# Kernel optimization log

Hardware: AMD Instinct MI355X
Metric: run time of the kernel (lower is better)

Reference implementation:

```python
import jax, jax.numpy as jnp
import numpy as np

B, T, D, H, O = 16, 2048, 512, 512, 256  # batch, max seq len, input, hidden, output


def setup_inputs() -> dict:
    key = jax.random.key(0)
    ks = jax.random.split(key, 12)
    x = jax.random.normal(ks[0], (B, T, D), dtype=jnp.float32)
    # ragged lengths: zero-pad the tail of each sample (zero rows => masked out)
    lengths = jax.random.randint(ks[1], (B,), T // 4, T + 1)
    valid = jnp.arange(T)[None, :] < lengths[:, None]
    x = x * valid[:, :, None].astype(x.dtype)
    s = float(1.0 / np.sqrt(H))  # PyTorch LSTM init range
    u = lambda k, shape: jax.random.uniform(k, shape, jnp.float32, -s, s)
    return {
        "x": x,
        "W_ih0": u(ks[2], (4 * H, D)), "W_hh0": u(ks[3], (4 * H, H)),
        "b_ih0": u(ks[4], (4 * H,)),   "b_hh0": u(ks[5], (4 * H,)),
        "W_ih1": u(ks[6], (4 * H, H)), "W_hh1": u(ks[7], (4 * H, H)),
        "b_ih1": u(ks[8], (4 * H,)),   "b_hh1": u(ks[9], (4 * H,)),
        "W_fc": u(ks[10], (O, H)),     "b_fc": u(ks[11], (O,)),
    }


def _lstm_layer(seq, mask, Wih, Whh, bih, bhh):
    """Masked LSTM layer over full batch.

    Skipping masked steps (state carried through unchanged) is mathematically
    identical to running the LSTM on the filtered (non-zero-row) subsequence,
    which is what the original per-sample Python loop computes.
    seq: [B, T, in], mask: [B, T] bool. Returns (outputs [B,T,H], h_final [B,H]).
    """
    Bn, Hn = seq.shape[0], Whh.shape[1]
    h0 = jnp.zeros((Bn, Hn), seq.dtype)
    c0 = jnp.zeros((Bn, Hn), seq.dtype)

    def step(carry, inp):
        h, c = carry
        x_t, m_t = inp
        gates = x_t @ Wih.T + bih + h @ Whh.T + bhh  # [B, 4H]
        i, f, g, o = jnp.split(gates, 4, axis=-1)    # PyTorch gate order i,f,g,o
        i = jax.nn.sigmoid(i)
        f = jax.nn.sigmoid(f)
        g = jnp.tanh(g)
        o = jax.nn.sigmoid(o)
        c_new = f * c + i * g
        h_new = o * jnp.tanh(c_new)
        m = m_t[:, None]
        h = jnp.where(m, h_new, h)
        c = jnp.where(m, c_new, c)
        return (h, c), h

    (hT, _), outs = jax.lax.scan(step, (h0, c0), (seq.transpose(1, 0, 2), mask.T))
    return outs.transpose(1, 0, 2), hT


def reference(x, W_ih0, W_hh0, b_ih0, b_hh0, W_ih1, W_hh1, b_ih1, b_hh1, W_fc, b_fc):
    mask = jnp.sum(x, axis=2) != 0  # [B, T] rows kept by the original filter
    seq1, _ = _lstm_layer(x, mask, W_ih0, W_hh0, b_ih0, b_hh0)
    _, hT = _lstm_layer(seq1, mask, W_ih1, W_hh1, b_ih1, b_hh1)
    return hT @ W_fc.T + b_fc  # [B, O]
```

## Files before the change

kernel.cpp:

```cpp
#include <hip/hip_runtime.h>

typedef _Float16 h16;
typedef __attribute__((ext_vector_type(2))) _Float16 h16x2;
typedef __attribute__((ext_vector_type(4))) _Float16 h16x4;
typedef __attribute__((ext_vector_type(8))) _Float16 h16x8;
typedef __attribute__((ext_vector_type(4))) float    f32x4;
typedef __attribute__((ext_vector_type(4))) unsigned u32x4;
typedef __attribute__((ext_vector_type(2))) unsigned u32x2;

constexpr int B_  = 16;
constexpr int T_  = 2048;
constexpr int D_  = 512;
constexpr int H_  = 512;
constexpr int O_  = 256;
constexpr int G4_ = 2048;
constexpr int BT_ = B_ * T_;

__device__ __forceinline__ float sigm(float x)   { return 1.f / (1.f + __expf(-x)); }
__device__ __forceinline__ float tanh_f(float x) { return 1.f - 2.f / (1.f + __expf(2.f * x)); }

__device__ __forceinline__ u32x4 load_cg16(const unsigned* p) {
  u32x4 r;
  asm volatile("global_load_dwordx4 %0, %1, off sc0 sc1" : "=v"(r) : "v"(p) : "memory");
  return r;
}

__global__ void k_prep_x(const float* __restrict__ x, h16* __restrict__ Xh,
                         unsigned* __restrict__ maskbits) {
  const int row = blockIdx.x;
  const int b = row >> 11, t = row & 2047;
  const float2* xr = (const float2*)(x + (size_t)row * D_);
  float2 v = xr[threadIdx.x];
  h16x2 hv = { (h16)v.x, (h16)v.y };
  *(h16x2*)(Xh + (size_t)row * D_ + threadIdx.x * 2) = hv;
  float s = v.x + v.y;
  #pragma unroll
  for (int off = 32; off > 0; off >>= 1) s += __shfl_down(s, off, 64);
  __shared__ float red[4];
  const int lane = threadIdx.x & 63, wv = threadIdx.x >> 6;
  if (lane == 0) red[wv] = s;
  __syncthreads();
  if (threadIdx.x == 0) {
    float tot = red[0] + red[1] + red[2] + red[3];
    if (tot != 0.f) atomicOr(&maskbits[t], 1u << b);
  }
}

__global__ void k_cvt(const float* __restrict__ s, h16* __restrict__ d, int n4) {
  int i = blockIdx.x * 256 + threadIdx.x;
  if (i < n4) {
    f32x4 v = ((const f32x4*)s)[i];
    h16x4 o = { (h16)v.x, (h16)v.y, (h16)v.z, (h16)v.w };
    ((h16x4*)d)[i] = o;
  }
}

__global__ void k_bias(const float* __restrict__ a, const float* __restrict__ b,
                       float* __restrict__ o, int n) {
  int i = blockIdx.x * 256 + threadIdx.x;
  if (i < n) o[i] = a[i] + b[i];
}

__global__ __launch_bounds__(256, 2)
void k_gemm(const h16* __restrict__ A, const h16* __restrict__ Bm, h16* __restrict__ C,
            int M, int N, int K) {
  __shared__ h16 As[128 * 32];
  __shared__ h16 Bs[128 * 32];
  const int tiles_n = N >> 7;
  const int tm = blockIdx.x / tiles_n, tn = blockIdx.x % tiles_n;
  const int tid = threadIdx.x, lane = tid & 63, wv = tid >> 6;
  const int wm = (wv >> 1) * 64, wn = (wv & 1) * 64;
  const int ml = lane & 15, qd = lane >> 4;
  f32x4 acc[4][4] = {};
  const h16* Arow = A + (size_t)(tm * 128) * K;
  const h16* Brow = Bm + (size_t)(tn * 128) * K;
  for (int kt = 0; kt < K; kt += 32) {
    __syncthreads();
    #pragma unroll
    for (int p = 0; p < 2; ++p) {
      int ch = tid + p * 256;
      int r = ch >> 2, qq = ch & 3;
      int sidx = r * 4 + ((qq + r) & 3);
      *(h16x8*)(As + sidx * 8) = *(const h16x8*)(Arow + (size_t)r * K + kt + qq * 8);
      *(h16x8*)(Bs + sidx * 8) = *(const h16x8*)(Brow + (size_t)r * K + kt + qq * 8);
    }
    __syncthreads();
    h16x8 af[4], bfv[4];
    #pragma unroll
    for (int i = 0; i < 4; ++i) {
      int ra = wm + i * 16 + ml;
      af[i]  = *(const h16x8*)(As + (ra * 4 + ((qd + ra) & 3)) * 8);
      int rb = wn + i * 16 + ml;
      bfv[i] = *(const h16x8*)(Bs + (rb * 4 + ((qd + rb) & 3)) * 8);
    }
    #pragma unroll
    for (int i = 0; i < 4; ++i)
      #pragma unroll
      for (int j = 0; j < 4; ++j)
        acc[i][j] = __builtin_amdgcn_mfma_f32_16x16x32_f16(af[i], bfv[j], acc[i][j], 0, 0, 0);
  }
  const int colb = lane & 15, rowq = (lane >> 4) * 4;
  #pragma unroll
  for (int i = 0; i < 4; ++i)
    #pragma unroll
    for (int j = 0; j < 4; ++j) {
      int row0 = tm * 128 + wm + i * 16 + rowq;
      int col  = tn * 128 + wn + j * 16 + colb;
      #pragma unroll
      for (int r = 0; r < 4; ++r)
        C[(size_t)(row0 + r) * N + col] = (h16)acc[i][j][r];
    }
}

__global__ __launch_bounds__(256, 1)
void k_lstm2m(const h16* __restrict__ G,
              const h16* __restrict__ Whh0,
              const h16* __restrict__ Wih1,
              const h16* __restrict__ Whh1,
              const float* __restrict__ bias0,
              const float* __restrict__ bias1,
              const unsigned* __restrict__ maskbits,
              unsigned* ring, float* hT_out) {
  const int g = blockIdx.x;
  const int tid = threadIdx.x, lane = tid & 63, w = tid >> 6;
  const int nl = lane & 15, qd = lane >> 4;

  __shared__ h16 Hst0[2][16 * 520];
  __shared__ h16 Hst1[2][16 * 520];
  __shared__ float ge0[4][16][18];
  __shared__ float ge1[4][16][18];
  __shared__ float c0s[16][17], c1s[16][17];

  h16x8 a_hh0[16], a_ih1[16], a_hh1[16];
  {
    const size_t ro = (size_t)(w * 512 + g * 16 + nl) * 512 + qd * 8;
    const h16* p0 = Whh0 + ro;
    const h16* p1 = Wih1 + ro;
    const h16* p2 = Whh1 + ro;
    #pragma unroll
    for (int kt = 0; kt < 16; ++kt) {
      a_hh0[kt] = *(const h16x8*)(p0 + kt * 32);
      a_ih1[kt] = *(const h16x8*)(p1 + kt * 32);
      a_hh1[kt] = *(const h16x8*)(p2 + kt * 32);
    }
  }
  float b0v[4], b1v[4];
  #pragma unroll
  for (int rr = 0; rr < 4; ++rr) {
    b0v[rr] = bias0[w * 512 + g * 16 + qd * 4 + rr];
    b1v[rr] = bias1[w * 512 + g * 16 + qd * 4 + rr];
  }

  for (int i = tid; i < 16 * 520; i += 256) {
    Hst0[0][i] = (h16)0.f; Hst0[1][i] = (h16)0.f;
    Hst1[0][i] = (h16)0.f; Hst1[1][i] = (h16)0.f;
  }
  const int jj = tid & 15, n = tid >> 4;
  c0s[jj][n] = 0.f;
  c1s[jj][n] = 0.f;
  __syncthreads();

  for (int r = 0; r <= T_; ++r) {
    const int buf = r & 1;
    h16x4 gv = {};
    if (r < T_)
      gv = *(const h16x4*)(G + ((size_t)nl * T_ + r) * G4_ + w * 512 + g * 16 + qd * 4);
    const unsigned mcur  = (r < T_) ? maskbits[r] : 0u;
    const unsigned mprev = (r > 0) ? maskbits[r - 1] : 0u;

    if (r > 0) {
      const unsigned tagw = (unsigned)r << 16;
      const unsigned* sb = ring + ((size_t)(r & 3) << 14) + tid * 4;
      h16* dst = (tid < 128) ? (Hst0[buf] + tid * 4) : (Hst1[buf] + (tid - 128) * 4);
      bool done = false;
      while (!done) {
        u32x4 v[16];
        #pragma unroll
        for (int j = 0; j < 16; ++j) v[j] = load_cg16(sb + j * 1024);
        asm volatile("s_waitcnt vmcnt(0)" ::: "memory");
        __builtin_amdgcn_sched_barrier(0);
        unsigned bad = 0;
        #pragma unroll
        for (int j = 0; j < 16; ++j)
          bad |= (v[j].x ^ tagw) | (v[j].y ^ tagw) | (v[j].z ^ tagw) | (v[j].w ^ tagw);
        if ((bad & 0xffff0000u) == 0) {
          #pragma unroll
          for (int j = 0; j < 16; ++j) {
            u32x2 pk;
            pk.x = (v[j].x & 0xffffu) | (v[j].y << 16);
            pk.y = (v[j].z & 0xffffu) | (v[j].w << 16);
            *(u32x2*)(dst + (size_t)j * 520) = pk;
          }
          done = true;
        }
      }
      __syncthreads();
    }

    f32x4 acc0 = {}, acc1a = {}, acc1b = {};
    if (r > 0) {
      const h16* h0p = Hst0[buf] + nl * 520 + qd * 8;
      const h16* h1p = Hst1[buf] + nl * 520 + qd * 8;
      #pragma unroll
      for (int kt = 0; kt < 16; ++kt) {
        h16x8 bb0 = *(const h16x8*)(h0p + kt * 32);
        if (r < T_) acc0 = __builtin_amdgcn_mfma_f32_16x16x32_f16(a_hh0[kt], bb0, acc0, 0, 0, 0);
        acc1a = __builtin_amdgcn_mfma_f32_16x16x32_f16(a_ih1[kt], bb0, acc1a, 0, 0, 0);
        h16x8 bb1 = *(const h16x8*)(h1p + kt * 32);
        acc1b = __builtin_amdgcn_mfma_f32_16x16x32_f16(a_hh1[kt], bb1, acc1b, 0, 0, 0);
      }
    }

    if (r < T_) {
      #pragma unroll
      for (int rr = 0; rr < 4; ++rr) {
        float pre = acc0[rr] + b0v[rr] + (float)gv[rr];
        ge0[w][qd * 4 + rr][nl] = (w == 2) ? tanh_f(pre) : sigm(pre);
      }
    }
    if (r > 0) {
      #pragma unroll
      for (int rr = 0; rr < 4; ++rr) {
        float pre = acc1a[rr] + acc1b[rr] + b1v[rr];
        ge1[w][qd * 4 + rr][nl] = (w == 2) ? tanh_f(pre) : sigm(pre);
      }
    }
    __syncthreads();

    {
      unsigned* slot = ring + (((size_t)((r + 1) & 3)) << 14) + (size_t)n * 1024 + g * 16 + jj;
      if (r < T_) {
        float iv = ge0[0][jj][n], fv = ge0[1][jj][n];
        float gg = ge0[2][jj][n], ov = ge0[3][jj][n];
        bool m = (mcur >> n) & 1u;
        float c_old = c0s[jj][n];
        float c_new = m ? (fv * c_old + iv * gg) : c_old;
        c0s[jj][n] = c_new;
        float h_old = (float)Hst0[buf][n * 520 + g * 16 + jj];
        float h_new = m ? (ov * tanh_f(c_new)) : h_old;
        h16 hh = (h16)h_new; unsigned short hb; __builtin_memcpy(&hb, &hh, 2);
        __hip_atomic_store(slot, ((unsigned)(r + 1) << 16) | hb,
                           __ATOMIC_RELAXED, __HIP_MEMORY_SCOPE_AGENT);
      }
      float h1_new = 0.f;
      if (r > 0) {
        float iv = ge1[0][jj][n], fv = ge1[1][jj][n];
        float gg = ge1[2][jj][n], ov = ge1[3][jj][n];
        bool m = (mprev >> n) & 1u;
        float c_old = c1s[jj][n];
        float c_new = m ? (fv * c_old + iv * gg) : c_old;
        c1s[jj][n] = c_new;
        float h_old = (float)Hst1[buf][n * 520 + g * 16 + jj];
        h1_new = m ? (ov * tanh_f(c_new)) : h_old;
      }
      if (r < T_) {
        h16 hh = (h16)h1_new; unsigned short hb; __builtin_memcpy(&hb, &hh, 2);
        __hip_atomic_store(slot + 512, ((unsigned)(r + 1) << 16) | hb,
                           __ATOMIC_RELAXED, __HIP_MEMORY_SCOPE_AGENT);
      } else {
        hT_out[(size_t)n * H_ + g * 16 + jj] = h1_new;
      }
    }
  }
}

__global__ void k_fc(const float* __restrict__ hT, const float* __restrict__ Wfc,
                     const float* __restrict__ bfc, float* __restrict__ out) {
  const int b = blockIdx.x;
  __shared__ float hs[H_];
  for (int i = threadIdx.x; i < H_; i += 256) hs[i] = hT[(size_t)b * H_ + i];
  __syncthreads();
  const int o = threadIdx.x;
  const float* wr = Wfc + (size_t)o * H_;
  float s = bfc[o];
  for (int k = 0; k < H_; k += 4) {
    f32x4 w4 = *(const f32x4*)(wr + k);
    s += hs[k] * w4.x + hs[k + 1] * w4.y + hs[k + 2] * w4.z + hs[k + 3] * w4.w;
  }
  out[(size_t)b * O_ + o] = s;
}

extern "C" void kernel_launch(void* const* d_in, const int* in_sizes, int n_in,
                              void* d_out, int out_size, void* d_ws, size_t ws_size,
                              hipStream_t stream) {
  const float* x    = (const float*)d_in[0];
  const float* Wih0 = (const float*)d_in[1];
  const float* Whh0 = (const float*)d_in[2];
  const float* bih0 = (const float*)d_in[3];
  const float* bhh0 = (const float*)d_in[4];
  const float* Wih1 = (const float*)d_in[5];
  const float* Whh1 = (const float*)d_in[6];
  const float* bih1 = (const float*)d_in[7];
  const float* bhh1 = (const float*)d_in[8];
  const float* Wfc  = (const float*)d_in[9];
  const float* bfc  = (const float*)d_in[10];

  char* base = (char*)d_ws;
  size_t off = 0;
  auto alloc = [&](size_t bytes) -> void* {
    void* r = base + off;
    off = (off + bytes + 255) & ~(size_t)255;
    return r;
  };
  h16* Xh   = (h16*)alloc((size_t)BT_ * D_ * 2);
  h16* Gbuf = (h16*)alloc((size_t)BT_ * G4_ * 2);
  h16* Wb0  = (h16*)alloc((size_t)G4_ * D_ * 2);
  h16* Wb1  = (h16*)alloc((size_t)G4_ * H_ * 2);
  h16* Wb2  = (h16*)alloc((size_t)G4_ * H_ * 2);
  h16* Wb3  = (h16*)alloc((size_t)G4_ * H_ * 2);
  float* bs0 = (float*)alloc(G4_ * 4);
  float* bs1 = (float*)alloc(G4_ * 4);
  unsigned* maskbits = (unsigned*)alloc(T_ * 4);
  unsigned* ring  = (unsigned*)alloc((size_t)4 * 16 * 1024 * 4);
  float* hT = (float*)alloc((size_t)B_ * H_ * 4);

  hipMemsetAsync(maskbits, 0, T_ * 4, stream);
  hipMemsetAsync(ring, 0, (size_t)4 * 16 * 1024 * 4, stream);
  k_prep_x<<<BT_, 256, 0, stream>>>(x, Xh, maskbits);
  const int wn4 = G4_ * D_ / 4;
  k_cvt<<<(wn4 + 255) / 256, 256, 0, stream>>>(Wih0, Wb0, wn4);
  k_cvt<<<(wn4 + 255) / 256, 256, 0, stream>>>(Whh0, Wb1, wn4);
  k_cvt<<<(wn4 + 255) / 256, 256, 0, stream>>>(Wih1, Wb2, wn4);
  k_cvt<<<(wn4 + 255) / 256, 256, 0, stream>>>(Whh1, Wb3, wn4);
  k_bias<<<(G4_ + 255) / 256, 256, 0, stream>>>(bih0, bhh0, bs0, G4_);
  k_bias<<<(G4_ + 255) / 256, 256, 0, stream>>>(bih1, bhh1, bs1, G4_);

  k_gemm<<<(BT_ / 128) * (G4_ / 128), 256, 0, stream>>>(Xh, Wb0, Gbuf, BT_, G4_, D_);
  k_lstm2m<<<32, 256, 0, stream>>>(Gbuf, Wb1, Wb2, Wb3, bs0, bs1, maskbits,
                                   ring, hT);
  k_fc<<<B_, 256, 0, stream>>>(hT, Wfc, bfc, (float*)d_out);
}
```

Before: 7.556 ms.

## Split fused LSTM step into layer phases with prefetched ring polling

```diff
diff --git a/kernel.cpp b/kernel.cpp
--- a/kernel.cpp
+++ b/kernel.cpp
@@ -22,6 +22,11 @@
 __device__ __forceinline__ u32x4 load_cg16(const unsigned* p) {
   u32x4 r;
   asm volatile("global_load_dwordx4 %0, %1, off sc0 sc1" : "=v"(r) : "v"(p) : "memory");
+  return r;
+}
+__device__ __forceinline__ u32x2 load_g8(const h16* p) {
+  u32x2 r;
+  asm volatile("global_load_dwordx2 %0, %1, off" : "=v"(r) : "v"(p) : "memory");
   return r;
 }
 
@@ -113,7 +118,7 @@
 }
 
 __global__ __launch_bounds__(256, 1)
-void k_lstm2m(const h16* __restrict__ G,
+void k_lstm2p(const h16* __restrict__ G,
               const h16* __restrict__ Whh0,
               const h16* __restrict__ Wih1,
               const h16* __restrict__ Whh1,
@@ -125,8 +130,8 @@
   const int tid = threadIdx.x, lane = tid & 63, w = tid >> 6;
   const int nl = lane & 15, qd = lane >> 4;
 
-  __shared__ h16 Hst0[2][16 * 520];
-  __shared__ h16 Hst1[2][16 * 520];
+  __shared__ h16 Hst0[2][16 * 512];
+  __shared__ h16 Hst1[2][16 * 512];
   __shared__ float ge0[4][16][18];
   __shared__ float ge1[4][16][18];
   __shared__ float c0s[16][17], c1s[16][17];
@@ -151,7 +156,7 @@
     b1v[rr] = bias1[w * 512 + g * 16 + qd * 4 + rr];
   }
 
-  for (int i = tid; i < 16 * 520; i += 256) {
+  for (int i = tid; i < 16 * 512; i += 256) {
     Hst0[0][i] = (h16)0.f; Hst0[1][i] = (h16)0.f;
     Hst1[0][i] = (h16)0.f; Hst1[1][i] = (h16)0.f;
   }
@@ -160,88 +165,148 @@
   c1s[jj][n] = 0.f;
   __syncthreads();
 
+  const int gn  = tid >> 7;
+  const int gcb = (tid & 127) * 4;
+  const int ukt = gcb >> 5, ukk = gcb & 31;
+  const int hkt = (g * 16 + jj) >> 5, hkk = (g * 16 + jj) & 31;
+
+  u32x4 pf0[8], pf1[8];
+  u32x2 gvr;
+  int budget = 1 << 22;
+
+  gvr = load_g8(G + ((size_t)nl * T_) * G4_ + w * 512 + g * 16 + qd * 4);
+
   for (int r = 0; r <= T_; ++r) {
     const int buf = r & 1;
-    h16x4 gv = {};
-    if (r < T_)
-      gv = *(const h16x4*)(G + ((size_t)nl * T_ + r) * G4_ + w * 512 + g * 16 + qd * 4);
     const unsigned mcur  = (r < T_) ? maskbits[r] : 0u;
     const unsigned mprev = (r > 0) ? maskbits[r - 1] : 0u;
 
     if (r > 0) {
       const unsigned tagw = (unsigned)r << 16;
-      const unsigned* sb = ring + ((size_t)(r & 3) << 14) + tid * 4;
-      h16* dst = (tid < 128) ? (Hst0[buf] + tid * 4) : (Hst1[buf] + (tid - 128) * 4);
-      bool done = false;
-      while (!done) {
-        u32x4 v[16];
+      const unsigned* sb = ring + ((size_t)(r & 3) << 14);
+      asm volatile("s_waitcnt vmcnt(1)" ::: "memory");
+      __builtin_amdgcn_sched_barrier(0);
+      for (;;) {
+        unsigned bad = 0;
         #pragma unroll
-        for (int j = 0; j < 16; ++j) v[j] = load_cg16(sb + j * 1024);
+        for (int j = 0; j < 8; ++j)
+          bad |= (pf0[j].x ^ tagw) | (pf0[j].y ^ tagw) | (pf0[j].z ^ tagw) | (pf0[j].w ^ tagw);
+        if (!(bad & 0xffff0000u)) break;
+        if (--budget < 0) break;
+        #pragma unroll
+        for (int j = 0; j < 8; ++j)
+          pf0[j] = load_cg16(sb + ((size_t)(gn + 2 * j) << 10) + gcb);
         asm volatile("s_waitcnt vmcnt(0)" ::: "memory");
         __builtin_amdgcn_sched_barrier(0);
+      }
+      #pragma unroll
+      for (int j = 0; j < 8; ++j) {
+        u32x2 pk;
+        pk.x = (pf0[j].x & 0xffffu) | (pf0[j].y << 16);
+        pk.y = (pf0[j].z & 0xffffu) | (pf0[j].w << 16);
+        *(u32x2*)(&Hst0[buf][ukt * 512 + (gn + 2 * j) * 32 + ukk]) = pk;
+      }
+    }
+    __syncthreads();
+    if (r > 0) {
+      const unsigned* sb = ring + ((size_t)(r & 3) << 14);
+      #pragma unroll
+      for (int j = 0; j < 8; ++j)
+        pf1[j] = load_cg16(sb + ((size_t)(gn + 2 * j) << 10) + 512 + gcb);
+    }
+    f32x4 a0a = {}, a0b = {};
+    if (r > 0 && r < T_) {
+      const h16* h0p = Hst0[buf] + nl * 32 + qd * 8;
+      #pragma unroll
+      for (int kt = 0; kt < 8; ++kt) {
+        h16x8 bb0 = *(const h16x8*)(h0p + kt * 512);
+        h16x8 bb1 = *(const h16x8*)(h0p + (kt + 8) * 512);
+        a0a = __builtin_amdgcn_mfma_f32_16x16x32_f16(a_hh0[kt],     bb0, a0a, 0, 0, 0);
+        a0b = __builtin_amdgcn_mfma_f32_16x16x32_f16(a_hh0[kt + 8], bb1, a0b, 0, 0, 0);
+      }
+    }
+    if (r == 0) {
+      asm volatile("s_waitcnt vmcnt(0)" ::: "memory");
+      __builtin_amdgcn_sched_barrier(0);
+    }
+    if (r < T_) {
+      h16x4 gv; __builtin_memcpy(&gv, &gvr, 8);
+      #pragma unroll
+      for (int rr = 0; rr < 4; ++rr) {
+        float pre = a0a[rr] + a0b[rr] + b0v[rr] + (float)gv[rr];
+        ge0[w][qd * 4 + rr][nl] = (w == 2) ? tanh_f(pre) : sigm(pre);
+      }
+    }
+    __syncthreads();
+    if (r < T_) {
+      float iv = ge0[0][jj][n], fv = ge0[1][jj][n];
+      float gg = ge0[2][jj][n], ov = ge0[3][jj][n];
+      bool m = (mcur >> n) & 1u;
+      float c_old = c0s[jj][n];
+      float c_new = m ? (fv * c_old + iv * gg) : c_old;
+      c0s[jj][n] = c_new;
+      float h_old = (float)Hst0[buf][hkt * 512 + n * 32 + hkk];
+      float h_new = m ? (ov * tanh_f(c_new)) : h_old;
+      h16 hh = (h16)h_new; unsigned short hb; __builtin_memcpy(&hb, &hh, 2);
+      __hip_atomic_store(ring + (((size_t)((r + 1) & 3)) << 14) + (size_t)n * 1024 + g * 16 + jj,
+                         ((unsigned)(r + 1) << 16) | hb,
+                         __ATOMIC_RELAXED, __HIP_MEMORY_SCOPE_AGENT);
+    }
+    if (r > 0) {
+      const unsigned tagw = (unsigned)r << 16;
+      const unsigned* sb = ring + ((size_t)(r & 3) << 14);
+      if (r < T_) asm volatile("s_waitcnt vmcnt(1)" ::: "memory");
+      else        asm volatile("s_waitcnt vmcnt(0)" ::: "memory");
+      __builtin_amdgcn_sched_barrier(0);
+      for (;;) {
         unsigned bad = 0;
         #pragma unroll
-        for (int j = 0; j < 16; ++j)
-          bad |= (v[j].x ^ tagw) | (v[j].y ^ tagw) | (v[j].z ^ tagw) | (v[j].w ^ tagw);
-        if ((bad & 0xffff0000u) == 0) {
-          #pragma unroll
-          for (int j = 0; j < 16; ++j) {
-            u32x2 pk;
-            pk.x = (v[j].x & 0xffffu) | (v[j].y << 16);
-            pk.y = (v[j].z & 0xffffu) | (v[j].w << 16);
-            *(u32x2*)(dst + (size_t)j * 520) = pk;
-          }
-          done = true;
-        }
-      }
-      __syncthreads();
-    }
-
-    f32x4 acc0 = {}, acc1a = {}, acc1b = {};
+        for (int j = 0; j < 8; ++j)
+          bad |= (pf1[j].x ^ tagw) | (pf1[j].y ^ tagw) | (pf1[j].z ^ tagw) | (pf1[j].w ^ tagw);
+        if (!(bad & 0xffff0000u)) break;
+        if (--budget < 0) break;
+        #pragma unroll
+        for (int j = 0; j < 8; ++j)
+          pf1[j] = load_cg16(sb + ((size_t)(gn + 2 * j) << 10) + 512 + gcb);
+        asm volatile("s_waitcnt vmcnt(0)" ::: "memory");
+        __builtin_amdgcn_sched_barrier(0);
+      }
+      #pragma unroll
+      for (int j = 0; j < 8; ++j) {
+        u32x2 pk;
+        pk.x = (pf1[j].x & 0xffffu) | (pf1[j].y << 16);
+        pk.y = (pf1[j].z & 0xffffu) | (pf1[j].w << 16);
+        *(u32x2*)(&Hst1[buf][ukt * 512 + (gn + 2 * j) * 32 + ukk]) = pk;
+      }
+    }
+    __syncthreads();
+    f32x4 a1a = {}, a1b = {};
     if (r > 0) {
-      const h16* h0p = Hst0[buf] + nl * 520 + qd * 8;
-      const h16* h1p = Hst1[buf] + nl * 520 + qd * 8;
+      const h16* h0p = Hst0[buf] + nl * 32 + qd * 8;
+      const h16* h1p = Hst1[buf] + nl * 32 + qd * 8;
       #pragma unroll
       for (int kt = 0; kt < 16; ++kt) {
-        h16x8 bb0 = *(const h16x8*)(h0p + kt * 32);
-        if (r < T_) acc0 = __builtin_amdgcn_mfma_f32_16x16x32_f16(a_hh0[kt], bb0, acc0, 0, 0, 0);
-        acc1a = __builtin_amdgcn_mfma_f32_16x16x32_f16(a_ih1[kt], bb0, acc1a, 0, 0, 0);
-        h16x8 bb1 = *(const h16x8*)(h1p + kt * 32);
-        acc1b = __builtin_amdgcn_mfma_f32_16x16x32_f16(a_hh1[kt], bb1, acc1b, 0, 0, 0);
-      }
-    }
-
+        h16x8 bb0 = *(const h16x8*)(h0p + kt * 512);
+        a1a = __builtin_amdgcn_mfma_f32_16x16x32_f16(a_ih1[kt], bb0, a1a, 0, 0, 0);
+        h16x8 bb1 = *(const h16x8*)(h1p + kt * 512);
+        a1b = __builtin_amdgcn_mfma_f32_16x16x32_f16(a_hh1[kt], bb1, a1b, 0, 0, 0);
+      }
+      #pragma unroll
+      for (int rr = 0; rr < 4; ++rr) {
+        float pre = a1a[rr] + a1b[rr] + b1v[rr];
+        ge1[w][qd * 4 + rr][nl] = (w == 2) ? tanh_f(pre) : sigm(pre);
+      }
+    }
+    __syncthreads();
     if (r < T_) {
-      #pragma unroll
-      for (int rr = 0; rr < 4; ++rr) {
-        float pre = acc0[rr] + b0v[rr] + (float)gv[rr];
-        ge0[w][qd * 4 + rr][nl] = (w == 2) ? tanh_f(pre) : sigm(pre);
-      }
-    }
-    if (r > 0) {
-      #pragma unroll
-      for (int rr = 0; rr < 4; ++rr) {
-        float pre = acc1a[rr] + acc1b[rr] + b1v[rr];
-        ge1[w][qd * 4 + rr][nl] = (w == 2) ? tanh_f(pre) : sigm(pre);
-      }
-    }
-    __syncthreads();
-
+      const unsigned* sb2 = ring + ((size_t)((r + 1) & 3) << 14);
+      #pragma unroll
+      for (int j = 0; j < 8; ++j)
+        pf0[j] = load_cg16(sb2 + ((size_t)(gn + 2 * j) << 10) + gcb);
+      if (r + 1 < T_)
+        gvr = load_g8(G + ((size_t)nl * T_ + (r + 1)) * G4_ + w * 512 + g * 16 + qd * 4);
+    }
     {
-      unsigned* slot = ring + (((size_t)((r + 1) & 3)) << 14) + (size_t)n * 1024 + g * 16 + jj;
-      if (r < T_) {
-        float iv = ge0[0][jj][n], fv = ge0[1][jj][n];
-        float gg = ge0[2][jj][n], ov = ge0[3][jj][n];
-        bool m = (mcur >> n) & 1u;
-        float c_old = c0s[jj][n];
-        float c_new = m ? (fv * c_old + iv * gg) : c_old;
-        c0s[jj][n] = c_new;
-        float h_old = (float)Hst0[buf][n * 520 + g * 16 + jj];
-        float h_new = m ? (ov * tanh_f(c_new)) : h_old;
-        h16 hh = (h16)h_new; unsigned short hb; __builtin_memcpy(&hb, &hh, 2);
-        __hip_atomic_store(slot, ((unsigned)(r + 1) << 16) | hb,
-                           __ATOMIC_RELAXED, __HIP_MEMORY_SCOPE_AGENT);
-      }
       float h1_new = 0.f;
       if (r > 0) {
         float iv = ge1[0][jj][n], fv = ge1[1][jj][n];
@@ -250,12 +315,13 @@
         float c_old = c1s[jj][n];
         float c_new = m ? (fv * c_old + iv * gg) : c_old;
         c1s[jj][n] = c_new;
-        float h_old = (float)Hst1[buf][n * 520 + g * 16 + jj];
+        float h_old = (float)Hst1[buf][hkt * 512 + n * 32 + hkk];
         h1_new = m ? (ov * tanh_f(c_new)) : h_old;
       }
       if (r < T_) {
         h16 hh = (h16)h1_new; unsigned short hb; __builtin_memcpy(&hb, &hh, 2);
-        __hip_atomic_store(slot + 512, ((unsigned)(r + 1) << 16) | hb,
+        __hip_atomic_store(ring + (((size_t)((r + 1) & 3)) << 14) + (size_t)n * 1024 + 512 + g * 16 + jj,
+                           ((unsigned)(r + 1) << 16) | hb,
                            __ATOMIC_RELAXED, __HIP_MEMORY_SCOPE_AGENT);
       } else {
         hT_out[(size_t)n * H_ + g * 16 + jj] = h1_new;
@@ -326,7 +392,7 @@
   k_bias<<<(G4_ + 255) / 256, 256, 0, stream>>>(bih1, bhh1, bs1, G4_);
 
   k_gemm<<<(BT_ / 128) * (G4_ / 128), 256, 0, stream>>>(Xh, Wb0, Gbuf, BT_, G4_, D_);
-  k_lstm2m<<<32, 256, 0, stream>>>(Gbuf, Wb1, Wb2, Wb3, bs0, bs1, maskbits,
+  k_lstm2p<<<32, 256, 0, stream>>>(Gbuf, Wb1, Wb2, Wb3, bs0, bs1, maskbits,
                                    ring, hT);
   k_fc<<<B_, 256, 0, stream>>>(hT, Wfc, bfc, (float*)d_out);
 }
```

Measured after the change: 8.102 ms. +7.2%, slower.

## Split persistent LSTM over 16 blocks of 512 threads with new hidden-state layout

Applied to the files above, without the earlier changes.

```diff
diff --git a/kernel.cpp b/kernel.cpp
--- a/kernel.cpp
+++ b/kernel.cpp
@@ -112,8 +112,8 @@
     }
 }
 
-__global__ __launch_bounds__(256, 1)
-void k_lstm2m(const h16* __restrict__ G,
+__global__ __launch_bounds__(512, 2)
+void k_lstm2w(const h16* __restrict__ G,
               const h16* __restrict__ Whh0,
               const h16* __restrict__ Wih1,
               const h16* __restrict__ Whh1,
@@ -122,18 +122,19 @@
               const unsigned* __restrict__ maskbits,
               unsigned* ring, float* hT_out) {
   const int g = blockIdx.x;
-  const int tid = threadIdx.x, lane = tid & 63, w = tid >> 6;
+  const int tid = threadIdx.x, lane = tid & 63, W = tid >> 6;
   const int nl = lane & 15, qd = lane >> 4;
-
-  __shared__ h16 Hst0[2][16 * 520];
-  __shared__ h16 Hst1[2][16 * 520];
-  __shared__ float ge0[4][16][18];
-  __shared__ float ge1[4][16][18];
-  __shared__ float c0s[16][17], c1s[16][17];
+  const int gate = W >> 1, colh = (W & 1) * 16;
+
+  __shared__ h16 Hst0[2][8192];
+  __shared__ h16 Hst1[2][8192];
+  __shared__ float ge0[4][32][17];
+  __shared__ float ge1[4][32][17];
+  __shared__ float c0s[32][17], c1s[32][17];
 
   h16x8 a_hh0[16], a_ih1[16], a_hh1[16];
   {
-    const size_t ro = (size_t)(w * 512 + g * 16 + nl) * 512 + qd * 8;
+    const size_t ro = (size_t)(gate * 512 + g * 32 + colh + nl) * 512 + qd * 8;
     const h16* p0 = Whh0 + ro;
     const h16* p1 = Wih1 + ro;
     const h16* p2 = Whh1 + ro;
@@ -147,66 +148,74 @@
   float b0v[4], b1v[4];
   #pragma unroll
   for (int rr = 0; rr < 4; ++rr) {
-    b0v[rr] = bias0[w * 512 + g * 16 + qd * 4 + rr];
-    b1v[rr] = bias1[w * 512 + g * 16 + qd * 4 + rr];
-  }
-
-  for (int i = tid; i < 16 * 520; i += 256) {
+    b0v[rr] = bias0[gate * 512 + g * 32 + colh + qd * 4 + rr];
+    b1v[rr] = bias1[gate * 512 + g * 32 + colh + qd * 4 + rr];
+  }
+
+  for (int i = tid; i < 8192; i += 512) {
     Hst0[0][i] = (h16)0.f; Hst0[1][i] = (h16)0.f;
     Hst1[0][i] = (h16)0.f; Hst1[1][i] = (h16)0.f;
   }
-  const int jj = tid & 15, n = tid >> 4;
+  const int jj = tid & 31, n = tid >> 5;
   c0s[jj][n] = 0.f;
   c1s[jj][n] = 0.f;
   __syncthreads();
+
+  const int t4 = tid * 4;
+  int budget = 1 << 22;
 
   for (int r = 0; r <= T_; ++r) {
     const int buf = r & 1;
     h16x4 gv = {};
     if (r < T_)
-      gv = *(const h16x4*)(G + ((size_t)nl * T_ + r) * G4_ + w * 512 + g * 16 + qd * 4);
+      gv = *(const h16x4*)(G + ((size_t)nl * T_ + r) * G4_
+                           + gate * 512 + g * 32 + colh + qd * 4);
     const unsigned mcur  = (r < T_) ? maskbits[r] : 0u;
     const unsigned mprev = (r > 0) ? maskbits[r - 1] : 0u;
 
     if (r > 0) {
       const unsigned tagw = (unsigned)r << 16;
-      const unsigned* sb = ring + ((size_t)(r & 3) << 14) + tid * 4;
-      h16* dst = (tid < 128) ? (Hst0[buf] + tid * 4) : (Hst1[buf] + (tid - 128) * 4);
+      const unsigned* sb = ring + ((size_t)(r & 3) << 14);
+      u32x4 v[8];
       bool done = false;
-      while (!done) {
-        u32x4 v[16];
+      while (!done && budget > 0) {
         #pragma unroll
-        for (int j = 0; j < 16; ++j) v[j] = load_cg16(sb + j * 1024);
+        for (int j = 0; j < 8; ++j) {
+          const int x = ((j & 3) << 11) + t4;
+          const int w0 = (((x >> 5) & 15) << 10) + ((j >> 2) << 9)
+                       + ((x >> 9) << 5) + (x & 31);
+          v[j] = load_cg16(sb + w0);
+        }
         asm volatile("s_waitcnt vmcnt(0)" ::: "memory");
         __builtin_amdgcn_sched_barrier(0);
         unsigned bad = 0;
         #pragma unroll
-        for (int j = 0; j < 16; ++j)
+        for (int j = 0; j < 8; ++j)
           bad |= (v[j].x ^ tagw) | (v[j].y ^ tagw) | (v[j].z ^ tagw) | (v[j].w ^ tagw);
-        if ((bad & 0xffff0000u) == 0) {
-          #pragma unroll
-          for (int j = 0; j < 16; ++j) {
-            u32x2 pk;
-            pk.x = (v[j].x & 0xffffu) | (v[j].y << 16);
-            pk.y = (v[j].z & 0xffffu) | (v[j].w << 16);
-            *(u32x2*)(dst + (size_t)j * 520) = pk;
-          }
-          done = true;
-        }
-      }
-      __syncthreads();
-    }
+        done = ((bad & 0xffff0000u) == 0);
+        --budget;
+      }
+      #pragma unroll
+      for (int j = 0; j < 8; ++j) {
+        u32x2 pk;
+        pk.x = (v[j].x & 0xffffu) | (v[j].y << 16);
+        pk.y = (v[j].z & 0xffffu) | (v[j].w << 16);
+        h16* dst = (j < 4 ? Hst0[buf] : Hst1[buf]) + ((j & 3) << 11) + t4;
+        *(u32x2*)dst = pk;
+      }
+    }
+    __syncthreads();
 
     f32x4 acc0 = {}, acc1a = {}, acc1b = {};
     if (r > 0) {
-      const h16* h0p = Hst0[buf] + nl * 520 + qd * 8;
-      const h16* h1p = Hst1[buf] + nl * 520 + qd * 8;
+      const h16* h0p = Hst0[buf] + nl * 32 + qd * 8;
+      const h16* h1p = Hst1[buf] + nl * 32 + qd * 8;
       #pragma unroll
       for (int kt = 0; kt < 16; ++kt) {
-        h16x8 bb0 = *(const h16x8*)(h0p + kt * 32);
+        h16x8 bb0 = *(const h16x8*)(h0p + kt * 512);
         if (r < T_) acc0 = __builtin_amdgcn_mfma_f32_16x16x32_f16(a_hh0[kt], bb0, acc0, 0, 0, 0);
         acc1a = __builtin_amdgcn_mfma_f32_16x16x32_f16(a_ih1[kt], bb0, acc1a, 0, 0, 0);
-        h16x8 bb1 = *(const h16x8*)(h1p + kt * 32);
+        h16x8 bb1 = *(const h16x8*)(h1p + kt * 512);
         acc1b = __builtin_amdgcn_mfma_f32_16x16x32_f16(a_hh1[kt], bb1, acc1b, 0, 0, 0);
       }
     }
@@ -215,20 +224,21 @@
       #pragma unroll
       for (int rr = 0; rr < 4; ++rr) {
         float pre = acc0[rr] + b0v[rr] + (float)gv[rr];
-        ge0[w][qd * 4 + rr][nl] = (w == 2) ? tanh_f(pre) : sigm(pre);
+        ge0[gate][colh + qd * 4 + rr][nl] = (gate == 2) ? tanh_f(pre) : sigm(pre);
       }
     }
     if (r > 0) {
       #pragma unroll
       for (int rr = 0; rr < 4; ++rr) {
         float pre = acc1a[rr] + acc1b[rr] + b1v[rr];
-        ge1[w][qd * 4 + rr][nl] = (w == 2) ? tanh_f(pre) : sigm(pre);
+        ge1[gate][colh + qd * 4 + rr][nl] = (gate == 2) ? tanh_f(pre) : sigm(pre);
       }
     }
     __syncthreads();
 
     {
-      unsigned* slot = ring + (((size_t)((r + 1) & 3)) << 14) + (size_t)n * 1024 + g * 16 + jj;
+      unsigned* slot = ring + (((size_t)((r + 1) & 3)) << 14)
+                     + (size_t)n * 1024 + g * 32 + jj;
       if (r < T_) {
         float iv = ge0[0][jj][n], fv = ge0[1][jj][n];
         float gg = ge0[2][jj][n], ov = ge0[3][jj][n];
@@ -236,7 +246,7 @@
         float c_old = c0s[jj][n];
         float c_new = m ? (fv * c_old + iv * gg) : c_old;
         c0s[jj][n] = c_new;
-        float h_old = (float)Hst0[buf][n * 520 + g * 16 + jj];
+        float h_old = (float)Hst0[buf][g * 512 + n * 32 + jj];
         float h_new = m ? (ov * tanh_f(c_new)) : h_old;
         h16 hh = (h16)h_new; unsigned short hb; __builtin_memcpy(&hb, &hh, 2);
         __hip_atomic_store(slot, ((unsigned)(r + 1) << 16) | hb,
@@ -250,7 +260,7 @@
         float c_old = c1s[jj][n];
         float c_new = m ? (fv * c_old + iv * gg) : c_old;
         c1s[jj][n] = c_new;
-        float h_old = (float)Hst1[buf][n * 520 + g * 16 + jj];
+        float h_old = (float)Hst1[buf][g * 512 + n * 32 + jj];
         h1_new = m ? (ov * tanh_f(c_new)) : h_old;
       }
       if (r < T_) {
@@ -258,7 +268,7 @@
         __hip_atomic_store(slot + 512, ((unsigned)(r + 1) << 16) | hb,
                            __ATOMIC_RELAXED, __HIP_MEMORY_SCOPE_AGENT);
       } else {
-        hT_out[(size_t)n * H_ + g * 16 + jj] = h1_new;
+        hT_out[(size_t)n * H_ + g * 32 + jj] = h1_new;
       }
     }
   }
@@ -326,7 +336,7 @@
   k_bias<<<(G4_ + 255) / 256, 256, 0, stream>>>(bih1, bhh1, bs1, G4_);
 
   k_gemm<<<(BT_ / 128) * (G4_ / 128), 256, 0, stream>>>(Xh, Wb0, Gbuf, BT_, G4_, D_);
-  k_lstm2m<<<32, 256, 0, stream>>>(Gbuf, Wb1, Wb2, Wb3, bs0, bs1, maskbits,
+  k_lstm2w<<<16, 512, 0, stream>>>(Gbuf, Wb1, Wb2, Wb3, bs0, bs1, maskbits,
                                    ring, hT);
   k_fc<<<B_, 256, 0, stream>>>(hT, Wfc, bfc, (float*)d_out);
 }
```

Result: slower. 10.73 ms (+42.1%).
